# Kernel optimization log

Hardware: AMD Instinct MI355X
Metric: run time of the kernel (lower is better)

The kernel has to match this reference:

```python
import jax, jax.numpy as jnp
import numpy as np

EPS = 1e-5

def _bn_relu(x, g, b, m, v):
    # inference batchnorm + relu, NCHW, fused affine
    scale = g * jax.lax.rsqrt(v + EPS)
    shift = b - m * scale
    return jnp.maximum(x * scale[None, :, None, None] + shift[None, :, None, None], 0.0)

def _conv1x1(x, w):
    # x: [B,C,H,W], w: [O,C]
    return jnp.einsum('bchw,oc->bohw', x, w)

def _xcorr_depthwise(search, kernel, padding=0):
    # search: [B,C,Hs,Ws], kernel: [B,C,Hk,Wk]; grouped conv, groups=B*C
    B, C, Hs, Ws = search.shape
    Hk, Wk = kernel.shape[2], kernel.shape[3]
    x = search.reshape(1, B * C, Hs, Ws)
    k = kernel.reshape(B * C, 1, Hk, Wk)
    out = jax.lax.conv_general_dilated(
        x, k, window_strides=(1, 1), padding=[(padding, padding), (padding, padding)],
        feature_group_count=B * C, dimension_numbers=('NCHW', 'OIHW', 'NCHW'))
    return out.reshape(B, C, out.shape[2], out.shape[3])

def setup_inputs():
    key = jax.random.key(0)
    ks = jax.random.split(key, 20)
    B, Cin, HID, COUT = 128, 256, 256, 20
    s = 1.0 / np.sqrt(Cin)
    inp = {
        'kernel': jax.random.normal(ks[0], (B, Cin, 7, 7), jnp.float32),
        'search': jax.random.normal(ks[1], (B, Cin, 31, 31), jnp.float32),
        # conv_kernel branch (1x1 conv weight stored as [O,C]) + BN stats
        'w_k': jax.random.normal(ks[2], (HID, Cin), jnp.float32) * s,
        'g_k': 1.0 + 0.1 * jax.random.normal(ks[3], (HID,), jnp.float32),
        'b_k': 0.1 * jax.random.normal(ks[4], (HID,), jnp.float32),
        'm_k': 0.1 * jax.random.normal(ks[5], (HID,), jnp.float32),
        'v_k': jax.random.uniform(ks[6], (HID,), jnp.float32, 0.5, 1.5),
        # conv_search branch
        'w_s': jax.random.normal(ks[7], (HID, Cin), jnp.float32) * s,
        'g_s': 1.0 + 0.1 * jax.random.normal(ks[8], (HID,), jnp.float32),
        'b_s': 0.1 * jax.random.normal(ks[9], (HID,), jnp.float32),
        'm_s': 0.1 * jax.random.normal(ks[10], (HID,), jnp.float32),
        'v_s': jax.random.uniform(ks[11], (HID,), jnp.float32, 0.5, 1.5),
        # head: conv1(1x1)+BN+ReLU, conv2(1x1, bias)
        'w_h1': jax.random.normal(ks[12], (HID, HID), jnp.float32) * (1.0 / np.sqrt(HID)),
        'g_h': 1.0 + 0.1 * jax.random.normal(ks[13], (HID,), jnp.float32),
        'b_h': 0.1 * jax.random.normal(ks[14], (HID,), jnp.float32),
        'm_h': 0.1 * jax.random.normal(ks[15], (HID,), jnp.float32),
        'v_h': jax.random.uniform(ks[16], (HID,), jnp.float32, 0.5, 1.5),
        'w_h2': jax.random.normal(ks[17], (COUT, HID), jnp.float32) * (1.0 / np.sqrt(HID)),
        'bias_h2': 0.1 * jax.random.normal(ks[18], (COUT,), jnp.float32),
    }
    return inp

def reference(kernel, search, w_k, g_k, b_k, m_k, v_k, w_s, g_s, b_s, m_s, v_s,
              w_h1, g_h, b_h, m_h, v_h, w_h2, bias_h2):
    k = _bn_relu(_conv1x1(kernel, w_k), g_k, b_k, m_k, v_k)   # [B,256,7,7]
    s = _bn_relu(_conv1x1(search, w_s), g_s, b_s, m_s, v_s)   # [B,256,31,31]
    feat = _xcorr_depthwise(s, k, padding=0)                  # [B,256,25,25]
    y = _bn_relu(_conv1x1(feat, w_h1), g_h, b_h, m_h, v_h)
    out = _conv1x1(y, w_h2) + bias_h2[None, :, None, None]    # [B,20,25,25]
    return out
```

## Files before the change

### kernel.cpp

```cpp
#include <hip/hip_runtime.h>
#include <hip/hip_fp16.h>

typedef _Float16 f16;
typedef __attribute__((ext_vector_type(8))) _Float16 f16x8;
typedef __attribute__((ext_vector_type(4))) _Float16 f16x4;
typedef __attribute__((ext_vector_type(2))) _Float16 f16x2;
typedef __attribute__((ext_vector_type(4))) float f32x4;

#define MFMA16(a, b, c) __builtin_amdgcn_mfma_f32_16x16x32_f16((a), (b), (c), 0, 0, 0)

#define OFF_WK   0u
#define OFF_WS   131072u
#define OFF_WH1  262144u
#define OFF_W2P  393216u
#define OFF_SH   409600u
#define OFF_S    412672u
#define OFF_KF   63392768u

__global__ __launch_bounds__(256) void prep_weights(
    const float* __restrict__ wk, const float* __restrict__ gk, const float* __restrict__ bk,
    const float* __restrict__ mk, const float* __restrict__ vk,
    const float* __restrict__ wsr, const float* __restrict__ gs, const float* __restrict__ bs,
    const float* __restrict__ ms, const float* __restrict__ vs,
    const float* __restrict__ wh1, const float* __restrict__ gh, const float* __restrict__ bh,
    const float* __restrict__ mh, const float* __restrict__ vh,
    const float* __restrict__ wh2,
    f16* __restrict__ wk16, f16* __restrict__ ws16, f16* __restrict__ wh116,
    f16* __restrict__ w2p, float* __restrict__ shifts) {
  int o = blockIdx.x;
  int t = threadIdx.x;
  float sck = gk[o] * rsqrtf(vk[o] + 1e-5f);
  float scs = gs[o] * rsqrtf(vs[o] + 1e-5f);
  float sch = gh[o] * rsqrtf(vh[o] + 1e-5f);
  int idx = o * 256 + t;
  wk16[idx]  = (f16)(wk[idx] * sck);
  ws16[idx]  = (f16)(wsr[idx] * scs);
  wh116[idx] = (f16)(wh1[idx] * sch);
  if (o < 32) w2p[idx] = (o < 20) ? (f16)wh2[idx] : (f16)0;
  if (t == 0) {
    shifts[o]       = bk[o] - mk[o] * sck;
    shifts[256 + o] = bs[o] - ms[o] * scs;
    shifts[512 + o] = bh[o] - mh[o] * sch;
  }
}

__device__ __forceinline__ int pi_row(int q, int r) {
  return (q ^ (r << 2)) + (r << 4);
}
__device__ __forceinline__ int row128(int n) {
  return (n & 64) + pi_row((n >> 2) & 15, n & 3);
}

__global__ __launch_bounds__(512) void conv_nchw128(
    const float* __restrict__ X, const f16* __restrict__ W,
    const float* __restrict__ shift, f16* __restrict__ out) {
  const int C = 256, P = 961;
  int b = blockIdx.x >> 3;
  int ti = blockIdx.x & 7;
  int n0 = ti * 128; if (n0 > P - 128) n0 = P - 128;
  int t = threadIdx.x;
  int w = t >> 6, lane = t & 63;
  int fm = lane & 15, kg = lane >> 4;
  int wo = (w & 3) * 64;
  int wpx = (w >> 2) * 64;

  __shared__ f16 Bs[2][128 * 40];

  int px = (t & 31) * 4;
  int cpr = (t >> 5) * 2;
  const float* xb = X + ((size_t)b * C) * P + n0 + px;

  int wrow[4];
#pragma unroll
  for (int e = 0; e < 4; ++e) wrow[e] = row128(px + e);
  int rrow[4];
#pragma unroll
  for (int nf = 0; nf < 4; ++nf) rrow[nf] = row128(wpx + nf * 16 + fm);

  const f16* wp = W + (size_t)(wo + fm) * C + kg * 8;

  f32x4 rb[3][2];
#pragma unroll
  for (int s = 0; s < 3; ++s) {
    int cl = s * 32 + cpr;
    rb[s][0] = *(const f32x4*)(xb + (size_t)cl * P);
    rb[s][1] = *(const f32x4*)(xb + (size_t)(cl + 1) * P);
  }

  f32x4 acc[4][4] = {};
#pragma unroll
  for (int ci = 0; ci < 8; ++ci) {
    f16x8 a[4];
#pragma unroll
    for (int of = 0; of < 4; ++of)
      a[of] = *(const f16x8*)(wp + (size_t)of * 16 * C + ci * 32);

    f16* buf = Bs[ci & 1];
#pragma unroll
    for (int e = 0; e < 4; ++e) {
      f16x2 v;
      v[0] = (f16)rb[ci % 3][0][e];
      v[1] = (f16)rb[ci % 3][1][e];
      *(f16x2*)&buf[wrow[e] * 40 + cpr] = v;
    }
    if (ci + 3 < 8) {
      int cl = (ci + 3) * 32 + cpr;
      rb[ci % 3][0] = *(const f32x4*)(xb + (size_t)cl * P);
      rb[ci % 3][1] = *(const f32x4*)(xb + (size_t)(cl + 1) * P);
    }
    asm volatile("s_waitcnt lgkmcnt(0)" ::: "memory");
    __builtin_amdgcn_s_barrier();

    f16x8 bfr[4];
#pragma unroll
    for (int nf = 0; nf < 4; ++nf)
      bfr[nf] = *(const f16x8*)&buf[rrow[nf] * 40 + kg * 8];
#pragma unroll
    for (int of = 0; of < 4; ++of)
#pragma unroll
      for (int nf = 0; nf < 4; ++nf)
        acc[of][nf] = MFMA16(a[of], bfr[nf], acc[of][nf]);
  }

#pragma unroll
  for (int of = 0; of < 4; ++of) {
    int orow = wo + of * 16 + kg * 4;
    f32x4 sh = *(const f32x4*)(shift + orow);
#pragma unroll
    for (int nf = 0; nf < 4; ++nf) {
      int n = n0 + wpx + nf * 16 + fm;
      f16x4 st;
#pragma unroll
      for (int r = 0; r < 4; ++r)
        st[r] = (f16)fmaxf(acc[of][nf][r] + sh[r], 0.0f);
      *(f16x4*)(out + ((size_t)b * P + n) * C + orow) = st;
    }
  }
}

template <int P>
__global__ __launch_bounds__(256) void conv_nchw(
    const float* __restrict__ X, const f16* __restrict__ W,
    const float* __restrict__ shift, f16* __restrict__ out) {
  const int C = 256;
  int n0 = blockIdx.x * 64;
  int t = threadIdx.x;
  int lane = t & 63, wave = t >> 6;
  int fm = lane & 15, kg = lane >> 4;

  __shared__ f16 Bs[2][64 * 40];

  int b0 = n0 / P, bp0 = n0 - b0 * P;
  bool safe = (bp0 + 64 <= P);

  int px = (t & 15) * 4;
  int cpr = (t >> 4) * 2;
  const float* xb = X + ((size_t)b0 * C) * P + bp0 + px;

  int ub[4], up[4];
  if (!safe) {
#pragma unroll
    for (int e = 0; e < 4; ++e) {
      int gn = n0 + px + e;
      ub[e] = gn / P;
      up[e] = gn - ub[e] * P;
    }
  }

  int wrow[4];
#pragma unroll
  for (int e = 0; e < 4; ++e) wrow[e] = pi_row(t & 15, e);
  int rrow[4];
#pragma unroll
  for (int nf = 0; nf < 4; ++nf) rrow[nf] = pi_row(nf * 4 + (fm >> 2), fm & 3);

  const f16* wp = W + (size_t)(wave * 64 + fm) * C + kg * 8;

  f32x4 rb[3][2];
#pragma unroll
  for (int s = 0; s < 3; ++s) {
    int cl = s * 32 + cpr;
    if (safe) {
      rb[s][0] = *(const f32x4*)(xb + (size_t)cl * P);
      rb[s][1] = *(const f32x4*)(xb + (size_t)(cl + 1) * P);
    } else {
#pragma unroll
      for (int e = 0; e < 4; ++e) {
        rb[s][0][e] = X[((size_t)ub[e] * C + cl) * P + up[e]];
        rb[s][1][e] = X[((size_t)ub[e] * C + cl + 1) * P + up[e]];
      }
    }
  }

  f32x4 acc[4][4] = {};
#pragma unroll
  for (int ci = 0; ci < 8; ++ci) {
    f16x8 a[4];
#pragma unroll
    for (int of = 0; of < 4; ++of)
      a[of] = *(const f16x8*)(wp + (size_t)of * 16 * C + ci * 32);

    f16* buf = Bs[ci & 1];
#pragma unroll
    for (int e = 0; e < 4; ++e) {
      f16x2 v;
      v[0] = (f16)rb[ci % 3][0][e];
      v[1] = (f16)rb[ci % 3][1][e];
      *(f16x2*)&buf[wrow[e] * 40 + cpr] = v;
    }
    if (ci + 3 < 8) {
      int cl = (ci + 3) * 32 + cpr;
      if (safe) {
        rb[ci % 3][0] = *(const f32x4*)(xb + (size_t)cl * P);
        rb[ci % 3][1] = *(const f32x4*)(xb + (size_t)(cl + 1) * P);
      } else {
#pragma unroll
        for (int e = 0; e < 4; ++e) {
          rb[ci % 3][0][e] = X[((size_t)ub[e] * C + cl) * P + up[e]];
          rb[ci % 3][1][e] = X[((size_t)ub[e] * C + cl + 1) * P + up[e]];
        }
      }
    }
    asm volatile("s_waitcnt lgkmcnt(0)" ::: "memory");
    __builtin_amdgcn_s_barrier();

    f16x8 b[4];
#pragma unroll
    for (int nf = 0; nf < 4; ++nf)
      b[nf] = *(const f16x8*)&buf[rrow[nf] * 40 + kg * 8];
#pragma unroll
    for (int of = 0; of < 4; ++of)
#pragma unroll
      for (int nf = 0; nf < 4; ++nf)
        acc[of][nf] = MFMA16(a[of], b[nf], acc[of][nf]);
  }

#pragma unroll
  for (int of = 0; of < 4; ++of) {
    int orow = wave * 64 + of * 16 + kg * 4;
    f32x4 sh = *(const f32x4*)(shift + orow);
#pragma unroll
    for (int nf = 0; nf < 4; ++nf) {
      int n = n0 + nf * 16 + fm;
      f16x4 st;
#pragma unroll
      for (int r = 0; r < 4; ++r)
        st[r] = (f16)fmaxf(acc[of][nf][r] + sh[r], 0.0f);
      *(f16x4*)(out + (size_t)n * C + orow) = st;
    }
  }
}

__global__ __launch_bounds__(256) void xcorr_head(
    const f16* __restrict__ S ,
    const f16* __restrict__ Kf ,
    const f16* __restrict__ W1, const float* __restrict__ shift,
    const f16* __restrict__ W2p, const float* __restrict__ bias,
    float* __restrict__ out ) {
  const int C = 256;
  int id = blockIdx.x;
  int x = id & 7;
  int r = id >> 3;
  int g = r % 7;
  int b = (r / 7) * 8 + x;

  int t = threadIdx.x;
  int w = t >> 6, lane = t & 63;
  int fm = lane & 15, kg = lane >> 4;
  int oi = g * 4 + w;

  __shared__ char F[100 * 512];

  if (oi < 25) {
    const f16* Sb = S + (size_t)b * 961 * 256 + lane * 4;
    const f16* Kb = Kf + (size_t)b * 49 * 256 + lane * 4;
    f16x4 acc[25] = {};
    for (int di = 0; di < 7; ++di) {
      const f16* sp = Sb + (size_t)(oi + di) * 31 * 256;
      f16x4 srow[31];
#pragma unroll
      for (int j = 0; j < 31; ++j) srow[j] = *(const f16x4*)(sp + (size_t)j * 256);
      const f16* kp = Kb + (size_t)di * 7 * 256;
      f16x4 krow[7];
#pragma unroll
      for (int j = 0; j < 7; ++j) krow[j] = *(const f16x4*)(kp + (size_t)j * 256);
#pragma unroll
      for (int dj = 0; dj < 7; ++dj) {
        f16x4 kv = krow[dj];
#pragma unroll
        for (int oj = 0; oj < 25; ++oj)
          acc[oj] += srow[oj + dj] * kv;
      }
    }
#pragma unroll
    for (int oj = 0; oj < 25; ++oj) {
      int n = w * 25 + oj;
      *(f16x4*)(F + ((n * 512 + lane * 8) ^ ((n & 7) << 4))) = acc[oj];
    }
  } else {
    f16x4 z = {};
#pragma unroll
    for (int oj = 0; oj < 25; ++oj) {
      int n = w * 25 + oj;
      *(f16x4*)(F + ((n * 512 + lane * 8) ^ ((n & 7) << 4))) = z;
    }
  }
  __syncthreads();

  const f16* wp = W1 + (size_t)(w * 64 + fm) * C + kg * 8;
  f32x4 acc1[4][7] = {};
#pragma unroll
  for (int ci = 0; ci < 8; ++ci) {
    f16x8 a[4];
#pragma unroll
    for (int of = 0; of < 4; ++of)
      a[of] = *(const f16x8*)(wp + (size_t)of * 16 * C + ci * 32);
    f16x8 bf[7];
#pragma unroll
    for (int nf = 0; nf < 7; ++nf) {
      int n = nf * 16 + fm;
      int rn = n < 100 ? n : n - 100;
      bf[nf] = *(const f16x8*)(F + ((rn * 512 + (ci * 32 + kg * 8) * 2) ^ ((rn & 7) << 4)));
    }
#pragma unroll
    for (int of = 0; of < 4; ++of)
#pragma unroll
      for (int nf = 0; nf < 7; ++nf)
        acc1[of][nf] = MFMA16(a[of], bf[nf], acc1[of][nf]);
  }
  __syncthreads();

#pragma unroll
  for (int of = 0; of < 4; ++of) {
    int orow = w * 64 + of * 16 + kg * 4;
    f32x4 sh = *(const f32x4*)(shift + orow);
#pragma unroll
    for (int nf = 0; nf < 7; ++nf) {
      int n = nf * 16 + fm;
      if (n < 100) {
        f16x4 st;
#pragma unroll
        for (int q = 0; q < 4; ++q)
          st[q] = (f16)fmaxf(acc1[of][nf][q] + sh[q], 0.0f);
        *(f16x4*)(F + ((n * 512 + orow * 2) ^ ((n & 7) << 4))) = st;
      }
    }
  }
  __syncthreads();

  f32x4 acc2[2][2] = {};
  int nfa = w, nfb = w + 4;
#pragma unroll
  for (int ci = 0; ci < 8; ++ci) {
    f16x8 a0 = *(const f16x8*)(W2p + (size_t)fm * C + ci * 32 + kg * 8);
    f16x8 a1 = *(const f16x8*)(W2p + (size_t)(16 + fm) * C + ci * 32 + kg * 8);
    int na = nfa * 16 + fm;
    f16x8 b0 = *(const f16x8*)(F + ((na * 512 + (ci * 32 + kg * 8) * 2) ^ ((na & 7) << 4)));
    acc2[0][0] = MFMA16(a0, b0, acc2[0][0]);
    acc2[1][0] = MFMA16(a1, b0, acc2[1][0]);
    if (nfb < 7) {
      int nb = nfb * 16 + fm;
      int rnb = nb < 100 ? nb : nb - 100;
      f16x8 b1 = *(const f16x8*)(F + ((rnb * 512 + (ci * 32 + kg * 8) * 2) ^ ((rnb & 7) << 4)));
      acc2[0][1] = MFMA16(a0, b1, acc2[0][1]);
      acc2[1][1] = MFMA16(a1, b1, acc2[1][1]);
    }
  }

#pragma unroll
  for (int q = 0; q < 2; ++q) {
    int nf = q ? nfb : nfa;
    if (nf >= 7) continue;
    int n = nf * 16 + fm;
    if (n < 100) {
      int oi2 = g * 4 + n / 25;
      int oj2 = n % 25;
      if (oi2 < 25) {
        float* op = out + (size_t)b * 12500 + oi2 * 25 + oj2;
#pragma unroll
        for (int of = 0; of < 2; ++of)
#pragma unroll
          for (int e = 0; e < 4; ++e) {
            int o = of * 16 + kg * 4 + e;
            if (o < 20) op[(size_t)o * 625] = acc2[of][q][e] + bias[o];
          }
      }
    }
  }
}

extern "C" void kernel_launch(void* const* d_in, const int* in_sizes, int n_in,
                              void* d_out, int out_size, void* d_ws, size_t ws_size,
                              hipStream_t stream) {
  const float* kernel_in = (const float*)d_in[0];
  const float* search    = (const float*)d_in[1];
  const float* w_k = (const float*)d_in[2];
  const float* g_k = (const float*)d_in[3];
  const float* b_k = (const float*)d_in[4];
  const float* m_k = (const float*)d_in[5];
  const float* v_k = (const float*)d_in[6];
  const float* w_s = (const float*)d_in[7];
  const float* g_s = (const float*)d_in[8];
  const float* b_s = (const float*)d_in[9];
  const float* m_s = (const float*)d_in[10];
  const float* v_s = (const float*)d_in[11];
  const float* w_h1 = (const float*)d_in[12];
  const float* g_h = (const float*)d_in[13];
  const float* b_h = (const float*)d_in[14];
  const float* m_h = (const float*)d_in[15];
  const float* v_h = (const float*)d_in[16];
  const float* w_h2 = (const float*)d_in[17];
  const float* bias_h2 = (const float*)d_in[18];
  float* out = (float*)d_out;

  char* ws = (char*)d_ws;
  f16* wk16  = (f16*)(ws + OFF_WK);
  f16* ws16  = (f16*)(ws + OFF_WS);
  f16* wh116 = (f16*)(ws + OFF_WH1);
  f16* w2p   = (f16*)(ws + OFF_W2P);
  float* shifts = (float*)(ws + OFF_SH);
  f16* sbuf = (f16*)(ws + OFF_S);
  f16* kbuf = (f16*)(ws + OFF_KF);

  prep_weights<<<256, 256, 0, stream>>>(w_k, g_k, b_k, m_k, v_k,
                                        w_s, g_s, b_s, m_s, v_s,
                                        w_h1, g_h, b_h, m_h, v_h, w_h2,
                                        wk16, ws16, wh116, w2p, shifts);

  conv_nchw128<<<dim3(1024), 512, 0, stream>>>(search, ws16, shifts + 256, sbuf);
  conv_nchw<49><<<dim3(98), 256, 0, stream>>>(kernel_in, wk16, shifts + 0, kbuf);

  xcorr_head<<<dim3(896), 256, 0, stream>>>(
      sbuf, kbuf, wh116, shifts + 512, w2p, bias_h2, out);
}
```

Measured before the change: 163.1 us.

## Split xcorr_head output columns into two halves to double block count

```diff
diff --git a/kernel.cpp b/kernel.cpp
--- a/kernel.cpp
+++ b/kernel.cpp
@@ -261,25 +261,31 @@
   int id = blockIdx.x;
   int x = id & 7;
   int r = id >> 3;
-  int g = r % 7;
-  int b = (r / 7) * 8 + x;
+  int h = r & 1;
+  int g = (r % 14) >> 1;
+  int b = (r / 14) * 8 + x;
 
   int t = threadIdx.x;
   int w = t >> 6, lane = t & 63;
   int fm = lane & 15, kg = lane >> 4;
   int oi = g * 4 + w;
-
-  __shared__ char F[100 * 512];
+  int oj0 = h * 13;
+
+  __shared__ char F[52 * 512];
 
   if (oi < 25) {
-    const f16* Sb = S + (size_t)b * 961 * 256 + lane * 4;
+    const f16* Sb = S + ((size_t)b * 961 + oj0) * 256 + lane * 4;
     const f16* Kb = Kf + (size_t)b * 49 * 256 + lane * 4;
-    f16x4 acc[25] = {};
+    f16x4 acc[13] = {};
     for (int di = 0; di < 7; ++di) {
       const f16* sp = Sb + (size_t)(oi + di) * 31 * 256;
-      f16x4 srow[31];
-#pragma unroll
-      for (int j = 0; j < 31; ++j) srow[j] = *(const f16x4*)(sp + (size_t)j * 256);
+      f16x4 srow[19];
+#pragma unroll
+      for (int j = 0; j < 19; ++j) {
+        int col = oj0 + j; col = col > 30 ? 30 : col;
+        srow[j] = *(const f16x4*)(sp + (size_t)(col - oj0) * 256 +
+                                  (size_t)(col - oj0 == j ? 0 : 0));
+      }
       const f16* kp = Kb + (size_t)di * 7 * 256;
       f16x4 krow[7];
 #pragma unroll
@@ -288,44 +294,44 @@
       for (int dj = 0; dj < 7; ++dj) {
         f16x4 kv = krow[dj];
 #pragma unroll
-        for (int oj = 0; oj < 25; ++oj)
-          acc[oj] += srow[oj + dj] * kv;
+        for (int ojl = 0; ojl < 13; ++ojl)
+          acc[ojl] += srow[ojl + dj] * kv;
       }
     }
 #pragma unroll
-    for (int oj = 0; oj < 25; ++oj) {
-      int n = w * 25 + oj;
-      *(f16x4*)(F + ((n * 512 + lane * 8) ^ ((n & 7) << 4))) = acc[oj];
+    for (int ojl = 0; ojl < 13; ++ojl) {
+      int n = w * 13 + ojl;
+      *(f16x4*)(F + ((n * 512 + lane * 8) ^ ((n & 7) << 4))) = acc[ojl];
     }
   } else {
     f16x4 z = {};
 #pragma unroll
-    for (int oj = 0; oj < 25; ++oj) {
-      int n = w * 25 + oj;
+    for (int ojl = 0; ojl < 13; ++ojl) {
+      int n = w * 13 + ojl;
       *(f16x4*)(F + ((n * 512 + lane * 8) ^ ((n & 7) << 4))) = z;
     }
   }
   __syncthreads();
 
   const f16* wp = W1 + (size_t)(w * 64 + fm) * C + kg * 8;
-  f32x4 acc1[4][7] = {};
+  f32x4 acc1[4][4] = {};
 #pragma unroll
   for (int ci = 0; ci < 8; ++ci) {
     f16x8 a[4];
 #pragma unroll
     for (int of = 0; of < 4; ++of)
       a[of] = *(const f16x8*)(wp + (size_t)of * 16 * C + ci * 32);
-    f16x8 bf[7];
-#pragma unroll
-    for (int nf = 0; nf < 7; ++nf) {
+    f16x8 bf[4];
+#pragma unroll
+    for (int nf = 0; nf < 4; ++nf) {
       int n = nf * 16 + fm;
-      int rn = n < 100 ? n : n - 100;
+      int rn = n < 52 ? n : n - 52;
       bf[nf] = *(const f16x8*)(F + ((rn * 512 + (ci * 32 + kg * 8) * 2) ^ ((rn & 7) << 4)));
     }
 #pragma unroll
     for (int of = 0; of < 4; ++of)
 #pragma unroll
-      for (int nf = 0; nf < 7; ++nf)
+      for (int nf = 0; nf < 4; ++nf)
         acc1[of][nf] = MFMA16(a[of], bf[nf], acc1[of][nf]);
   }
   __syncthreads();
@@ -335,9 +341,9 @@
     int orow = w * 64 + of * 16 + kg * 4;
     f32x4 sh = *(const f32x4*)(shift + orow);
 #pragma unroll
-    for (int nf = 0; nf < 7; ++nf) {
+    for (int nf = 0; nf < 4; ++nf) {
       int n = nf * 16 + fm;
-      if (n < 100) {
+      if (n < 52) {
         f16x4 st;
 #pragma unroll
         for (int q = 0; q < 4; ++q)
@@ -348,43 +354,31 @@
   }
   __syncthreads();
 
-  f32x4 acc2[2][2] = {};
-  int nfa = w, nfb = w + 4;
+  f32x4 acc2[2] = {};
+  int nfr = w * 16 + fm;
+  int rn3 = nfr < 52 ? nfr : nfr - 52;
 #pragma unroll
   for (int ci = 0; ci < 8; ++ci) {
     f16x8 a0 = *(const f16x8*)(W2p + (size_t)fm * C + ci * 32 + kg * 8);
     f16x8 a1 = *(const f16x8*)(W2p + (size_t)(16 + fm) * C + ci * 32 + kg * 8);
-    int na = nfa * 16 + fm;
-    f16x8 b0 = *(const f16x8*)(F + ((na * 512 + (ci * 32 + kg * 8) * 2) ^ ((na & 7) << 4)));
-    acc2[0][0] = MFMA16(a0, b0, acc2[0][0]);
-    acc2[1][0] = MFMA16(a1, b0, acc2[1][0]);
-    if (nfb < 7) {
-      int nb = nfb * 16 + fm;
-      int rnb = nb < 100 ? nb : nb - 100;
-      f16x8 b1 = *(const f16x8*)(F + ((rnb * 512 + (ci * 32 + kg * 8) * 2) ^ ((rnb & 7) << 4)));
-      acc2[0][1] = MFMA16(a0, b1, acc2[0][1]);
-      acc2[1][1] = MFMA16(a1, b1, acc2[1][1]);
-    }
-  }
-
-#pragma unroll
-  for (int q = 0; q < 2; ++q) {
-    int nf = q ? nfb : nfa;
-    if (nf >= 7) continue;
-    int n = nf * 16 + fm;
-    if (n < 100) {
-      int oi2 = g * 4 + n / 25;
-      int oj2 = n % 25;
-      if (oi2 < 25) {
-        float* op = out + (size_t)b * 12500 + oi2 * 25 + oj2;
-#pragma unroll
-        for (int of = 0; of < 2; ++of)
-#pragma unroll
-          for (int e = 0; e < 4; ++e) {
-            int o = of * 16 + kg * 4 + e;
-            if (o < 20) op[(size_t)o * 625] = acc2[of][q][e] + bias[o];
-          }
-      }
+    f16x8 b0 = *(const f16x8*)(F + ((rn3 * 512 + (ci * 32 + kg * 8) * 2) ^ ((rn3 & 7) << 4)));
+    acc2[0] = MFMA16(a0, b0, acc2[0]);
+    acc2[1] = MFMA16(a1, b0, acc2[1]);
+  }
+
+  if (nfr < 52) {
+    int oil = nfr / 13, ojl = nfr - oil * 13;
+    int oi2 = g * 4 + oil;
+    int oj2 = oj0 + ojl;
+    if (oi2 < 25 && oj2 < 25) {
+      float* op = out + (size_t)b * 12500 + oi2 * 25 + oj2;
+#pragma unroll
+      for (int of = 0; of < 2; ++of)
+#pragma unroll
+        for (int e = 0; e < 4; ++e) {
+          int o = of * 16 + kg * 4 + e;
+          if (o < 20) op[(size_t)o * 625] = acc2[of][e] + bias[o];
+        }
     }
   }
 }
@@ -430,6 +424,6 @@
   conv_nchw128<<<dim3(1024), 512, 0, stream>>>(search, ws16, shifts + 256, sbuf);
   conv_nchw<49><<<dim3(98), 256, 0, stream>>>(kernel_in, wk16, shifts + 0, kbuf);
 
-  xcorr_head<<<dim3(896), 256, 0, stream>>>(
+  xcorr_head<<<dim3(1792), 256, 0, stream>>>(
       sbuf, kbuf, wh116, shifts + 512, w2p, bias_h2, out);
 }
```

New measurement: 168.9 us. +3.6%, slower.
